# Kernel tuning notes

Hardware: AMD Instinct MI355X
Metric: run time of the kernel (lower is better)

Reference implementation:

```python
import jax, jax.numpy as jnp
import numpy as np

N_NODES = 50000
N_EDGES = 800000
IN_F = 128
OUT_F = 64
NEG_SLOPE = 0.2  # GATConv default leaky relu slope

def setup_inputs() -> dict:
    key = jax.random.key(0)
    k1, k2, k3, k4, k5 = jax.random.split(key, 5)
    x = jax.random.normal(k1, (N_NODES, IN_F), dtype=jnp.float32)
    edge_index = jax.random.randint(k2, (2, N_EDGES), 0, N_NODES, dtype=jnp.int64)
    W = jax.random.normal(k3, (IN_F, OUT_F), dtype=jnp.float32) * (1.0 / np.sqrt(IN_F))
    att_src = jax.random.normal(k4, (OUT_F,), dtype=jnp.float32) * 0.1
    att_dst = jax.random.normal(k5, (OUT_F,), dtype=jnp.float32) * 0.1
    bias = jnp.zeros((OUT_F,), dtype=jnp.float32)
    return {"x": x, "edge_index": edge_index, "W": W, "att_src": att_src, "att_dst": att_dst, "bias": bias}

def reference(x, edge_index, W, att_src, att_dst, bias):
    N = x.shape[0]
    h = x @ W  # [N, out]
    # GATConv adds self-loops by default
    loops = jnp.arange(N, dtype=edge_index.dtype)
    src = jnp.concatenate([edge_index[0], loops])  # message sources (neighbors j)
    dst = jnp.concatenate([edge_index[1], loops])  # targets i (softmax segments)
    a_src = h @ att_src  # [N]
    a_dst = h @ att_dst  # [N]
    e = a_src[src] + a_dst[dst]  # [E+N]
    e = jnp.where(e > 0, e, NEG_SLOPE * e)
    # segment softmax over incoming edges of each target node
    e_max = jax.ops.segment_max(e, dst, num_segments=N)
    p = jnp.exp(e - e_max[dst])
    denom = jax.ops.segment_sum(p, dst, num_segments=N)
    alpha = p / (denom[dst] + 1e-16)  # [E+N]
    # scatter-add aggregate weighted source features
    out = jax.ops.segment_sum(h[src] * alpha[:, None], dst, num_segments=N)  # [N, out]
    out = jax.nn.relu(out + bias)
    return out[None]  # wrapper unsqueezes: [1, N, out]
```

## Files before the change

### kernel.cpp

```cpp
#include <hip/hip_runtime.h>
#include <hip/hip_bf16.h>
#include <math.h>

#define N_NODES 50000
#define N_EDGES 800000
#define IN_F 128
#define OUT_F 64
#define NEG_SLOPE 0.2f

#define CAP 64
#define GB 196
#define TPW 4
#define PSZ 128
#define NPART ((N_NODES + PSZ - 1) / PSZ)
#define PADCAP 3072
#define CHUNK 2048
#define NCHUNK ((N_EDGES + CHUNK - 1) / CHUNK)

typedef __attribute__((ext_vector_type(8))) short bf16x8;
typedef __attribute__((ext_vector_type(4))) float f32x4;

__device__ __forceinline__ short f2bf_s(float f) {
    return (short)__builtin_bit_cast(unsigned short, __float2bfloat16(f));
}
__device__ __forceinline__ unsigned short f2bf_u(float f) {
    return __builtin_bit_cast(unsigned short, __float2bfloat16(f));
}
__device__ __forceinline__ float bf_lo(unsigned u) { return __uint_as_float(u << 16); }
__device__ __forceinline__ float bf_hi(unsigned u) { return __uint_as_float(u & 0xFFFF0000u); }

__global__ __launch_bounds__(256) void k_prep(
    const float* __restrict__ W, const float* __restrict__ att_src,
    const float* __restrict__ att_dst, unsigned short* __restrict__ wa,
    unsigned short* __restrict__ wd, int* __restrict__ gcnt) {
    int t = threadIdx.x;
    for (int i = t; i < NPART; i += 256) gcnt[i] = 0;
    if (t < IN_F) {
        float s1 = 0.f, s2 = 0.f;
        const float* wr = &W[t * OUT_F];
        for (int c = 0; c < OUT_F; ++c) {
            float wv = wr[c];
            s1 = fmaf(wv, att_src[c], s1);
            s2 = fmaf(wv, att_dst[c], s2);
        }
        wa[t] = f2bf_u(s1);
        wd[t] = f2bf_u(s2);
    }
}

__global__ __launch_bounds__(256) void k_fused(
    const float* __restrict__ x, const float* __restrict__ W,
    const unsigned short* __restrict__ wa, const unsigned short* __restrict__ wd,
    const int* __restrict__ ei, unsigned short* __restrict__ h,
    float* __restrict__ a_src, float* __restrict__ a_dst,
    int* __restrict__ gcnt, unsigned* __restrict__ glist) {
    int tid = threadIdx.x;

    if (blockIdx.x >= GB) {
        __shared__ int bcnt[NPART];
        __shared__ int bbase[NPART];
        int f = blockIdx.x - GB;
        for (int i = tid; i < NPART; i += 256) bcnt[i] = 0;
        __syncthreads();

        int e0 = f * CHUNK + tid * 8;
        bool val = e0 < N_EDGES;
        int sv[8], dv[8], sl[8];
        if (val) {
            const int4 sa = *reinterpret_cast<const int4*>(ei + e0);
            const int4 sb = *reinterpret_cast<const int4*>(ei + e0 + 4);
            const int4 da = *reinterpret_cast<const int4*>(ei + N_EDGES + e0);
            const int4 db = *reinterpret_cast<const int4*>(ei + N_EDGES + e0 + 4);
            sv[0]=sa.x; sv[1]=sa.y; sv[2]=sa.z; sv[3]=sa.w;
            sv[4]=sb.x; sv[5]=sb.y; sv[6]=sb.z; sv[7]=sb.w;
            dv[0]=da.x; dv[1]=da.y; dv[2]=da.z; dv[3]=da.w;
            dv[4]=db.x; dv[5]=db.y; dv[6]=db.z; dv[7]=db.w;
#pragma unroll
            for (int i = 0; i < 8; ++i)
                sl[i] = atomicAdd(&bcnt[dv[i] >> 7], 1);
        }
        __syncthreads();
        for (int i = tid; i < NPART; i += 256)
            bbase[i] = bcnt[i] ? atomicAdd(&gcnt[i], bcnt[i]) : 0;
        __syncthreads();
        if (val) {
#pragma unroll
            for (int i = 0; i < 8; ++i) {
                int p = dv[i] >> 7;
                int idx = bbase[p] + sl[i];
                if (idx < PADCAP)
                    glist[(size_t)p * PADCAP + idx] =
                        (unsigned)(sv[i] & 0xFFFF) | ((unsigned)(dv[i] & (PSZ - 1)) << 16);
            }
        }
        return;
    }

    int w = tid >> 6;
    int lane = tid & 63;
    int col = lane & 15;
    int kg = lane >> 4;
    int gw = blockIdx.x * 4 + w;

    bf16x8 bf[4][4];
#pragma unroll
    for (int ks = 0; ks < 4; ++ks)
#pragma unroll
        for (int nt = 0; nt < 4; ++nt) {
            bf16x8 b;
#pragma unroll
            for (int i = 0; i < 8; ++i)
                b[i] = f2bf_s(W[(ks * 32 + kg * 8 + i) * OUT_F + col * 4 + nt]);
            bf[ks][nt] = b;
        }
    bf16x8 bf5[4];
#pragma unroll
    for (int ks = 0; ks < 4; ++ks) {
        bf16x8 b = {0, 0, 0, 0, 0, 0, 0, 0};
        if (col == 0) b = *reinterpret_cast<const bf16x8*>(&wa[ks * 32 + kg * 8]);
        if (col == 1) b = *reinterpret_cast<const bf16x8*>(&wd[ks * 32 + kg * 8]);
        bf5[ks] = b;
    }

    for (int it = 0; it < TPW; ++it) {
        int r0 = (gw * TPW + it) * 16;
        if (r0 >= N_NODES) break;
        const float* xp = &x[(size_t)(r0 + col) * IN_F + kg * 8];

        bf16x8 af[4];
#pragma unroll
        for (int ks = 0; ks < 4; ++ks) {
            float4 xa = *reinterpret_cast<const float4*>(xp + ks * 32);
            float4 xb = *reinterpret_cast<const float4*>(xp + ks * 32 + 4);
            bf16x8 a;
            a[0] = f2bf_s(xa.x); a[1] = f2bf_s(xa.y);
            a[2] = f2bf_s(xa.z); a[3] = f2bf_s(xa.w);
            a[4] = f2bf_s(xb.x); a[5] = f2bf_s(xb.y);
            a[6] = f2bf_s(xb.z); a[7] = f2bf_s(xb.w);
            af[ks] = a;
        }

        f32x4 acc[4], acc5;
        f32x4 z = {0.f, 0.f, 0.f, 0.f};
#pragma unroll
        for (int nt = 0; nt < 4; ++nt) acc[nt] = z;
        acc5 = z;
#pragma unroll
        for (int ks = 0; ks < 4; ++ks) {
#pragma unroll
            for (int nt = 0; nt < 4; ++nt)
                acc[nt] = __builtin_amdgcn_mfma_f32_16x16x32_bf16(
                    af[ks], bf[ks][nt], acc[nt], 0, 0, 0);
            acc5 = __builtin_amdgcn_mfma_f32_16x16x32_bf16(
                af[ks], bf5[ks], acc5, 0, 0, 0);
        }

#pragma unroll
        for (int j = 0; j < 4; ++j) {
            int r = r0 + kg * 4 + j;
            ushort4 hv;
            hv.x = f2bf_u(acc[0][j]);
            hv.y = f2bf_u(acc[1][j]);
            hv.z = f2bf_u(acc[2][j]);
            hv.w = f2bf_u(acc[3][j]);
            *reinterpret_cast<ushort4*>(&h[(size_t)r * OUT_F + col * 4]) = hv;
        }
        if (col < 2) {
            float* ap = (col == 0) ? a_src : a_dst;
#pragma unroll
            for (int j = 0; j < 4; ++j) ap[r0 + kg * 4 + j] = acc5[j];
        }
    }
}

__global__ __launch_bounds__(1024) void k_csr_node(
    const int* __restrict__ gcnt, const unsigned* __restrict__ glist,
    const float* __restrict__ a_src, const float* __restrict__ a_dst,
    const unsigned short* __restrict__ h, const float* __restrict__ bias,
    float* __restrict__ out) {
    __shared__ unsigned short lcsr[PSZ][CAP];
    __shared__ int lcnt[PSZ];
    int p = blockIdx.x;
    int tid = threadIdx.x;
    int n0 = p * PSZ;

    for (int i = tid; i < PSZ; i += 1024) {
        lcnt[i] = 1;
        lcsr[i][0] = (unsigned short)(n0 + i);
    }
    __syncthreads();

    int m = min(gcnt[p], PADCAP);
    size_t base = (size_t)p * PADCAP;
    for (int i = tid; i < m; i += 1024) {
        unsigned u = glist[base + i];
        int dl = u >> 16;
        int k = atomicAdd(&lcnt[dl], 1);
        if (k < CAP) lcsr[dl][k] = (unsigned short)(u & 0xFFFFu);
    }
    __syncthreads();

    int w = tid >> 6;
    int lane = tid & 63;
    int half = lane >> 5;
    int hl = lane & 31;
    int es = hl >> 3;
    int cb = hl & 7;
    int hbase = half << 5;
    int nn_nodes = min(PSZ, N_NODES - n0);

    for (int it = 0; it < PSZ / 32; ++it) {
        int nl = it * 32 + w * 2 + half;
        if (nl >= nn_nodes) continue;
        int node = n0 + nl;
        int n = min(lcnt[nl], CAP);
        float a_d = a_dst[node];
        float acc8[8];
#pragma unroll
        for (int i = 0; i < 8; ++i) acc8[i] = 0.f;
        float l = 0.f;

        if (n <= 32) {
            int s = 0;
            float pp = 0.f;
            if (hl < n) {
                s = lcsr[nl][hl];
                float t = a_src[s] + a_d;
                t = (t > 0.f) ? t : NEG_SLOPE * t;
                pp = __expf(t);
            }
            l = pp;
            for (int off = 16; off; off >>= 1) l += __shfl_xor(l, off, 64);

            int jn = (n + 3) >> 2;
            for (int j = 0; j < jn; ++j) {
                int sl = j * 4 + es;
                float pj = __shfl(pp, hbase + sl, 64);
                int sj = __shfl(s, hbase + sl, 64);
                if (sl < n) {
                    uint4 hv =
                        *reinterpret_cast<const uint4*>(&h[(size_t)sj * OUT_F + cb * 8]);
                    acc8[0] = fmaf(pj, bf_lo(hv.x), acc8[0]);
                    acc8[1] = fmaf(pj, bf_hi(hv.x), acc8[1]);
                    acc8[2] = fmaf(pj, bf_lo(hv.y), acc8[2]);
                    acc8[3] = fmaf(pj, bf_hi(hv.y), acc8[3]);
                    acc8[4] = fmaf(pj, bf_lo(hv.z), acc8[4]);
                    acc8[5] = fmaf(pj, bf_hi(hv.z), acc8[5]);
                    acc8[6] = fmaf(pj, bf_lo(hv.w), acc8[6]);
                    acc8[7] = fmaf(pj, bf_hi(hv.w), acc8[7]);
                }
            }
        } else {
            for (int b2 = 0; b2 < n; b2 += 32) {
                int nn = min(32, n - b2);
                int s = 0;
                float pp = 0.f;
                if (hl < nn) {
                    s = lcsr[nl][b2 + hl];
                    float t = a_src[s] + a_d;
                    t = (t > 0.f) ? t : NEG_SLOPE * t;
                    pp = __expf(t);
                }
                float ps = pp;
                for (int off = 16; off; off >>= 1) ps += __shfl_xor(ps, off, 64);
                l += ps;

                int jn = (nn + 3) >> 2;
                for (int j = 0; j < jn; ++j) {
                    int sl = j * 4 + es;
                    float pj = __shfl(pp, hbase + sl, 64);
                    int sj = __shfl(s, hbase + sl, 64);
                    if (sl < nn) {
                        uint4 hv = *reinterpret_cast<const uint4*>(
                            &h[(size_t)sj * OUT_F + cb * 8]);
                        acc8[0] = fmaf(pj, bf_lo(hv.x), acc8[0]);
                        acc8[1] = fmaf(pj, bf_hi(hv.x), acc8[1]);
                        acc8[2] = fmaf(pj, bf_lo(hv.y), acc8[2]);
                        acc8[3] = fmaf(pj, bf_hi(hv.y), acc8[3]);
                        acc8[4] = fmaf(pj, bf_lo(hv.z), acc8[4]);
                        acc8[5] = fmaf(pj, bf_hi(hv.z), acc8[5]);
                        acc8[6] = fmaf(pj, bf_lo(hv.w), acc8[6]);
                        acc8[7] = fmaf(pj, bf_hi(hv.w), acc8[7]);
                    }
                }
            }
        }

#pragma unroll
        for (int i = 0; i < 8; ++i) {
            acc8[i] += __shfl_xor(acc8[i], 8, 64);
            acc8[i] += __shfl_xor(acc8[i], 16, 64);
        }

        if (hl < 8) {
            float inv = 1.f / (l + 1e-16f);
            const float4 b0 = *reinterpret_cast<const float4*>(&bias[cb * 8]);
            const float4 b1 = *reinterpret_cast<const float4*>(&bias[cb * 8 + 4]);
            float4 o0, o1;
            o0.x = fmaxf(acc8[0] * inv + b0.x, 0.f);
            o0.y = fmaxf(acc8[1] * inv + b0.y, 0.f);
            o0.z = fmaxf(acc8[2] * inv + b0.z, 0.f);
            o0.w = fmaxf(acc8[3] * inv + b0.w, 0.f);
            o1.x = fmaxf(acc8[4] * inv + b1.x, 0.f);
            o1.y = fmaxf(acc8[5] * inv + b1.y, 0.f);
            o1.z = fmaxf(acc8[6] * inv + b1.z, 0.f);
            o1.w = fmaxf(acc8[7] * inv + b1.w, 0.f);
            float* op = &out[(size_t)node * OUT_F + cb * 8];
            *reinterpret_cast<float4*>(op) = o0;
            *reinterpret_cast<float4*>(op + 4) = o1;
        }
    }
}

extern "C" void kernel_launch(void* const* d_in, const int* in_sizes, int n_in,
                              void* d_out, int out_size, void* d_ws, size_t ws_size,
                              hipStream_t stream) {
    const float* x       = (const float*)d_in[0];
    const int*   ei      = (const int*)d_in[1];
    const float* W       = (const float*)d_in[2];
    const float* att_src = (const float*)d_in[3];
    const float* att_dst = (const float*)d_in[4];
    const float* bias    = (const float*)d_in[5];
    float* out = (float*)d_out;

    char* wsp = (char*)d_ws;
    unsigned short* h = (unsigned short*)wsp;
    wsp += (size_t)N_NODES * OUT_F * sizeof(unsigned short);
    float* a_src = (float*)wsp; wsp += (size_t)N_NODES * sizeof(float);
    float* a_dst = (float*)wsp; wsp += (size_t)N_NODES * sizeof(float);
    int*   gcnt  = (int*)wsp;   wsp += (size_t)NPART * sizeof(int);
    wsp = (char*)(((size_t)wsp + 15) & ~(size_t)15);
    unsigned short* wa = (unsigned short*)wsp; wsp += IN_F * sizeof(unsigned short);
    unsigned short* wd = (unsigned short*)wsp; wsp += IN_F * sizeof(unsigned short);
    wsp = (char*)(((size_t)wsp + 15) & ~(size_t)15);
    unsigned* glist = (unsigned*)wsp;
    wsp += (size_t)NPART * PADCAP * sizeof(unsigned);

    hipLaunchKernelGGL(k_prep, dim3(1), dim3(256), 0, stream,
                       W, att_src, att_dst, wa, wd, gcnt);
    hipLaunchKernelGGL(k_fused, dim3(GB + NCHUNK), dim3(256), 0, stream,
                       x, W, wa, wd, ei, h, a_src, a_dst, gcnt, glist);
    hipLaunchKernelGGL(k_csr_node, dim3(NPART), dim3(1024), 0, stream,
                       gcnt, glist, a_src, a_dst, h, bias, out);
}
```

Before: 48.85 us.

## Fold prep kernel into fused GEMM and shrink node partitions to 64

Removes the single-block prep kernel. Each GEMM wave now computes W·att_src and W·att_dst itself with wavefront shuffles, and gcnt is zeroed with a memset instead. Node partitions shrink from 128 to 64 nodes, so the CSR kernel launches twice as many 512-thread blocks. Each binning block now handles 4096 edges with 16 per thread. The aim is to cut a serial launch and improve load balance and occupancy in the aggregation kernel, at the cost of redundant per-wave reductions and more partitions.

```diff
diff --git a/kernel.cpp b/kernel.cpp
--- a/kernel.cpp
+++ b/kernel.cpp
@@ -11,10 +11,10 @@
 #define CAP 64
 #define GB 196
 #define TPW 4
-#define PSZ 128
+#define PSZ 64
 #define NPART ((N_NODES + PSZ - 1) / PSZ)
-#define PADCAP 3072
-#define CHUNK 2048
+#define PADCAP 1664
+#define CHUNK 4096
 #define NCHUNK ((N_EDGES + CHUNK - 1) / CHUNK)
 
 typedef __attribute__((ext_vector_type(8))) short bf16x8;
@@ -29,28 +29,9 @@
 __device__ __forceinline__ float bf_lo(unsigned u) { return __uint_as_float(u << 16); }
 __device__ __forceinline__ float bf_hi(unsigned u) { return __uint_as_float(u & 0xFFFF0000u); }
 
-__global__ __launch_bounds__(256) void k_prep(
-    const float* __restrict__ W, const float* __restrict__ att_src,
-    const float* __restrict__ att_dst, unsigned short* __restrict__ wa,
-    unsigned short* __restrict__ wd, int* __restrict__ gcnt) {
-    int t = threadIdx.x;
-    for (int i = t; i < NPART; i += 256) gcnt[i] = 0;
-    if (t < IN_F) {
-        float s1 = 0.f, s2 = 0.f;
-        const float* wr = &W[t * OUT_F];
-        for (int c = 0; c < OUT_F; ++c) {
-            float wv = wr[c];
-            s1 = fmaf(wv, att_src[c], s1);
-            s2 = fmaf(wv, att_dst[c], s2);
-        }
-        wa[t] = f2bf_u(s1);
-        wd[t] = f2bf_u(s2);
-    }
-}
-
 __global__ __launch_bounds__(256) void k_fused(
     const float* __restrict__ x, const float* __restrict__ W,
-    const unsigned short* __restrict__ wa, const unsigned short* __restrict__ wd,
+    const float* __restrict__ att_src, const float* __restrict__ att_dst,
     const int* __restrict__ ei, unsigned short* __restrict__ h,
     float* __restrict__ a_src, float* __restrict__ a_dst,
     int* __restrict__ gcnt, unsigned* __restrict__ glist) {
@@ -63,21 +44,22 @@
         for (int i = tid; i < NPART; i += 256) bcnt[i] = 0;
         __syncthreads();
 
-        int e0 = f * CHUNK + tid * 8;
+        int e0 = f * CHUNK + tid * 16;
         bool val = e0 < N_EDGES;
-        int sv[8], dv[8], sl[8];
+        int sv[16], dv[16], sl[16];
         if (val) {
-            const int4 sa = *reinterpret_cast<const int4*>(ei + e0);
-            const int4 sb = *reinterpret_cast<const int4*>(ei + e0 + 4);
-            const int4 da = *reinterpret_cast<const int4*>(ei + N_EDGES + e0);
-            const int4 db = *reinterpret_cast<const int4*>(ei + N_EDGES + e0 + 4);
-            sv[0]=sa.x; sv[1]=sa.y; sv[2]=sa.z; sv[3]=sa.w;
-            sv[4]=sb.x; sv[5]=sb.y; sv[6]=sb.z; sv[7]=sb.w;
-            dv[0]=da.x; dv[1]=da.y; dv[2]=da.z; dv[3]=da.w;
-            dv[4]=db.x; dv[5]=db.y; dv[6]=db.z; dv[7]=db.w;
-#pragma unroll
-            for (int i = 0; i < 8; ++i)
-                sl[i] = atomicAdd(&bcnt[dv[i] >> 7], 1);
+#pragma unroll
+            for (int q = 0; q < 4; ++q) {
+                const int4 s4 = *reinterpret_cast<const int4*>(ei + e0 + q * 4);
+                const int4 d4 = *reinterpret_cast<const int4*>(ei + N_EDGES + e0 + q * 4);
+                sv[q * 4 + 0] = s4.x; sv[q * 4 + 1] = s4.y;
+                sv[q * 4 + 2] = s4.z; sv[q * 4 + 3] = s4.w;
+                dv[q * 4 + 0] = d4.x; dv[q * 4 + 1] = d4.y;
+                dv[q * 4 + 2] = d4.z; dv[q * 4 + 3] = d4.w;
+            }
+#pragma unroll
+            for (int i = 0; i < 16; ++i)
+                sl[i] = atomicAdd(&bcnt[dv[i] >> 6], 1);
         }
         __syncthreads();
         for (int i = tid; i < NPART; i += 256)
@@ -85,8 +67,8 @@
         __syncthreads();
         if (val) {
 #pragma unroll
-            for (int i = 0; i < 8; ++i) {
-                int p = dv[i] >> 7;
+            for (int i = 0; i < 16; ++i) {
+                int p = dv[i] >> 6;
                 int idx = bbase[p] + sl[i];
                 if (idx < PADCAP)
                     glist[(size_t)p * PADCAP + idx] =
@@ -102,24 +84,36 @@
     int kg = lane >> 4;
     int gw = blockIdx.x * 4 + w;
 
+    const float4 as4 = *reinterpret_cast<const float4*>(&att_src[col * 4]);
+    const float4 ad4 = *reinterpret_cast<const float4*>(&att_dst[col * 4]);
+
     bf16x8 bf[4][4];
-#pragma unroll
-    for (int ks = 0; ks < 4; ++ks)
-#pragma unroll
-        for (int nt = 0; nt < 4; ++nt) {
-            bf16x8 b;
-#pragma unroll
-            for (int i = 0; i < 8; ++i)
-                b[i] = f2bf_s(W[(ks * 32 + kg * 8 + i) * OUT_F + col * 4 + nt]);
-            bf[ks][nt] = b;
-        }
     bf16x8 bf5[4];
 #pragma unroll
     for (int ks = 0; ks < 4; ++ks) {
-        bf16x8 b = {0, 0, 0, 0, 0, 0, 0, 0};
-        if (col == 0) b = *reinterpret_cast<const bf16x8*>(&wa[ks * 32 + kg * 8]);
-        if (col == 1) b = *reinterpret_cast<const bf16x8*>(&wd[ks * 32 + kg * 8]);
-        bf5[ks] = b;
+        bf16x8 b0, b1, b2, b3;
+        float p1[8], p2[8];
+#pragma unroll
+        for (int i = 0; i < 8; ++i) {
+            const float4 w4 = *reinterpret_cast<const float4*>(
+                &W[(ks * 32 + kg * 8 + i) * OUT_F + col * 4]);
+            b0[i] = f2bf_s(w4.x); b1[i] = f2bf_s(w4.y);
+            b2[i] = f2bf_s(w4.z); b3[i] = f2bf_s(w4.w);
+            p1[i] = w4.x * as4.x + w4.y * as4.y + w4.z * as4.z + w4.w * as4.w;
+            p2[i] = w4.x * ad4.x + w4.y * ad4.y + w4.z * ad4.z + w4.w * ad4.w;
+        }
+        bf[ks][0] = b0; bf[ks][1] = b1; bf[ks][2] = b2; bf[ks][3] = b3;
+        bf16x8 w5 = {0, 0, 0, 0, 0, 0, 0, 0};
+#pragma unroll
+        for (int i = 0; i < 8; ++i) {
+            for (int off = 8; off; off >>= 1) {
+                p1[i] += __shfl_xor(p1[i], off, 64);
+                p2[i] += __shfl_xor(p2[i], off, 64);
+            }
+            if (col == 0) w5[i] = f2bf_s(p1[i]);
+            if (col == 1) w5[i] = f2bf_s(p2[i]);
+        }
+        bf5[ks] = w5;
     }
 
     for (int it = 0; it < TPW; ++it) {
@@ -173,7 +167,7 @@
     }
 }
 
-__global__ __launch_bounds__(1024) void k_csr_node(
+__global__ __launch_bounds__(512) void k_csr_node(
     const int* __restrict__ gcnt, const unsigned* __restrict__ glist,
     const float* __restrict__ a_src, const float* __restrict__ a_dst,
     const unsigned short* __restrict__ h, const float* __restrict__ bias,
@@ -184,7 +178,7 @@
     int tid = threadIdx.x;
     int n0 = p * PSZ;
 
-    for (int i = tid; i < PSZ; i += 1024) {
+    for (int i = tid; i < PSZ; i += 512) {
         lcnt[i] = 1;
         lcsr[i][0] = (unsigned short)(n0 + i);
     }
@@ -192,7 +186,7 @@
 
     int m = min(gcnt[p], PADCAP);
     size_t base = (size_t)p * PADCAP;
-    for (int i = tid; i < m; i += 1024) {
+    for (int i = tid; i < m; i += 512) {
         unsigned u = glist[base + i];
         int dl = u >> 16;
         int k = atomicAdd(&lcnt[dl], 1);
@@ -209,8 +203,8 @@
     int hbase = half << 5;
     int nn_nodes = min(PSZ, N_NODES - n0);
 
-    for (int it = 0; it < PSZ / 32; ++it) {
-        int nl = it * 32 + w * 2 + half;
+    for (int it = 0; it < PSZ / 16; ++it) {
+        int nl = it * 16 + w * 2 + half;
         if (nl >= nn_nodes) continue;
         int node = n0 + nl;
         int n = min(lcnt[nl], CAP);
@@ -330,16 +324,12 @@
     float* a_dst = (float*)wsp; wsp += (size_t)N_NODES * sizeof(float);
     int*   gcnt  = (int*)wsp;   wsp += (size_t)NPART * sizeof(int);
     wsp = (char*)(((size_t)wsp + 15) & ~(size_t)15);
-    unsigned short* wa = (unsigned short*)wsp; wsp += IN_F * sizeof(unsigned short);
-    unsigned short* wd = (unsigned short*)wsp; wsp += IN_F * sizeof(unsigned short);
-    wsp = (char*)(((size_t)wsp + 15) & ~(size_t)15);
     unsigned* glist = (unsigned*)wsp;
     wsp += (size_t)NPART * PADCAP * sizeof(unsigned);
 
-    hipLaunchKernelGGL(k_prep, dim3(1), dim3(256), 0, stream,
-                       W, att_src, att_dst, wa, wd, gcnt);
+    hipMemsetAsync(gcnt, 0, (size_t)NPART * sizeof(int), stream);
     hipLaunchKernelGGL(k_fused, dim3(GB + NCHUNK), dim3(256), 0, stream,
-                       x, W, wa, wd, ei, h, a_src, a_dst, gcnt, glist);
-    hipLaunchKernelGGL(k_csr_node, dim3(NPART), dim3(1024), 0, stream,
+                       x, W, att_src, att_dst, ei, h, a_src, a_dst, gcnt, glist);
+    hipLaunchKernelGGL(k_csr_node, dim3(NPART), dim3(512), 0, stream,
                        gcnt, glist, a_src, a_dst, h, bias, out);
 }
```

Measured after the change: 56.94 us. 1.17x slower.
